# Performance work log

Measured on AMD Instinct MI355X. Metric: run time of the kernel, lower is better.

Reference implementation:

```python
import jax, jax.numpy as jnp
import numpy as np

NUM_ENT = 100000
NUM_REL = 500            # distinct relations; table holds 2*NUM_REL (forward + inverse)
E = 500000               # total edges: first half original, second half reversed
D = 200                  # init_dim = gcn_dim = embed_dim
B = 256
KW, KH = 10, 20          # ConvE reshape: 2*KW*KH == 2*D
NF, KS = 200, 7
FLAT = (2 * KW - KS + 1) * (KH - KS + 1) * NF  # 14*14*200 = 39200
EPS = 1e-5


def setup_inputs() -> dict:
    key = jax.random.key(0)
    k = jax.random.split(key, 24)
    half = E // 2
    src = jax.random.randint(k[0], (half,), 0, NUM_ENT)
    dst = jax.random.randint(k[1], (half,), 0, NUM_ENT)
    et = jax.random.randint(k[2], (half,), 0, NUM_REL)
    edge_index = jnp.stack([jnp.concatenate([src, dst]), jnp.concatenate([dst, src])])
    edge_type = jnp.concatenate([et, et + NUM_REL])
    sub = jax.random.randint(k[3], (B,), 0, NUM_ENT)
    rel = jax.random.randint(k[4], (B,), 0, 2 * NUM_REL)
    g = lambda i, shape, s=0.05: jax.random.normal(k[i], shape, jnp.float32) * s
    return dict(
        sub=sub, rel=rel, edge_index=edge_index, edge_type=edge_type,
        init_embed=g(5, (NUM_ENT, D)), init_rel=g(6, (2 * NUM_REL, D)),
        loop_rel1=g(7, (1, D)), loop_rel2=g(8, (1, D)),
        w_in1=g(9, (D, D)), w_out1=g(10, (D, D)), w_loop1=g(11, (D, D)), w_rel1=g(12, (D, D)), b1=jnp.zeros((D,), jnp.float32),
        w_in2=g(13, (D, D)), w_out2=g(14, (D, D)), w_loop2=g(15, (D, D)), w_rel2=g(16, (D, D)), b2=jnp.zeros((D,), jnp.float32),
        conv_w=g(17, (NF, 1, KS, KS)), conv_b=jnp.zeros((NF,), jnp.float32),
        bn0_g=jnp.ones((1,), jnp.float32), bn0_b=jnp.zeros((1,), jnp.float32),
        bn1_g=jnp.ones((NF,), jnp.float32), bn1_b=jnp.zeros((NF,), jnp.float32),
        bn2_g=jnp.ones((D,), jnp.float32), bn2_b=jnp.zeros((D,), jnp.float32),
        fc_w=g(18, (FLAT, D)), fc_b=jnp.zeros((D,), jnp.float32),
        ent_bias=jnp.zeros((NUM_ENT,), jnp.float32),
    )


def _bn2d(x, g, b):  # eval-mode BN: running mean 0, running var 1
    s = g / jnp.sqrt(1.0 + EPS)
    return x * s[None, :, None, None] + b[None, :, None, None]


def _bn1d(x, g, b):
    return x * (g / jnp.sqrt(1.0 + EPS)) + b


def _agg(x_src, rel_e, dst, w):
    # message = comp(h_src, h_rel) @ W   (subtraction composition), degree-normalized scatter
    m = (x_src - rel_e) @ w                                        # [E/2, D]
    s = jax.ops.segment_sum(m, dst, num_segments=NUM_ENT)          # [N, D]
    deg = jax.ops.segment_sum(jnp.ones(dst.shape, m.dtype), dst, num_segments=NUM_ENT)
    return s / jnp.clip(deg, 1.0)[:, None]


def _ragcn_layer(x, r, ei, et, w_in, w_out, w_loop, w_rel, loop_rel, b):
    half = ei.shape[1] // 2
    src, dst = ei[0], ei[1]
    re = r[et]                                                     # [E, D]
    res = (_agg(x[src[:half]], re[:half], dst[:half], w_in)
           + _agg(x[src[half:]], re[half:], dst[half:], w_out)
           + (x - loop_rel) @ w_loop)
    return jnp.tanh(res / 3.0 + b), r @ w_rel


def _forward(sub, rel, edge_index, edge_type, init_embed, init_rel,
             loop_rel1, loop_rel2, w_in1, w_out1, w_loop1, w_rel1, b1,
             w_in2, w_out2, w_loop2, w_rel2, b2, conv_w, conv_b,
             bn0_g, bn0_b, bn1_g, bn1_b, bn2_g, bn2_b, fc_w, fc_b, ent_bias):
    x, r = _ragcn_layer(init_embed, init_rel, edge_index, edge_type, w_in1, w_out1, w_loop1, w_rel1, loop_rel1, b1)
    x, r = _ragcn_layer(x, r, edge_index, edge_type, w_in2, w_out2, w_loop2, w_rel2, loop_rel2, b2)
    sub_emb = x[sub]                                               # [B, D]
    rel_emb = r[rel]                                               # [B, D]
    # ConvE concat: [B,2,D] -> [B,D,2] -> [B,1,2*KW,KH]
    stk = jnp.transpose(jnp.stack([sub_emb, rel_emb], axis=1), (0, 2, 1)).reshape(-1, 1, 2 * KW, KH)
    h = _bn2d(stk, bn0_g, bn0_b)
    h = jax.lax.conv_general_dilated(h, conv_w, (1, 1), 'VALID',
                                     dimension_numbers=('NCHW', 'OIHW', 'NCHW'))
    h = h + conv_b[None, :, None, None]
    h = jax.nn.relu(_bn2d(h, bn1_g, bn1_b))
    h = h.reshape(-1, FLAT)
    h = h @ fc_w + fc_b
    h = jax.nn.relu(_bn1d(h, bn2_g, bn2_b))
    logits = h @ x.T + ent_bias                                    # [B, NUM_ENT]
    return jax.nn.sigmoid(logits)


def reference(sub, rel, edge_index, edge_type, init_embed, init_rel,
              loop_rel1, loop_rel2, w_in1, w_out1, w_loop1, w_rel1, b1,
              w_in2, w_out2, w_loop2, w_rel2, b2, conv_w, conv_b,
              bn0_g, bn0_b, bn1_g, bn1_b, bn2_g, bn2_b, fc_w, fc_b, ent_bias):
    return _forward(sub, rel, edge_index, edge_type, init_embed, init_rel,
                    loop_rel1, loop_rel2, w_in1, w_out1, w_loop1, w_rel1, b1,
                    w_in2, w_out2, w_loop2, w_rel2, b2, conv_w, conv_b,
                    bn0_g, bn0_b, bn1_g, bn1_b, bn2_g, bn2_b, fc_w, fc_b, ent_bias)
```

## Files before the change

### kernel.cpp

```cpp
#include <hip/hip_runtime.h>
#include <math.h>

#define N_ENT   100000
#define N_REL2  1000
#define E_TOT   500000
#define E_HALF  250000
#define DIM     200
#define BB      256
#define NFILT   200
#define FLATK   39200
#define EPS_BN  1e-5f

#define NROWS   200000
#define SCHUNK  2048
#define SNBLK   ((NROWS + SCHUNK - 1) / SCHUNK)

#define FC_KC   175
#define FC_KLEN 224

typedef __attribute__((ext_vector_type(8))) short bf16x8;
typedef __attribute__((ext_vector_type(4))) float f32x4;

__device__ __forceinline__ unsigned short f2b(float f) {
    union { float f; unsigned u; } c; c.f = f;
    unsigned u = c.u;
    u += 0x7fffu + ((u >> 16) & 1u);
    return (unsigned short)(u >> 16);
}
__device__ __forceinline__ float b2f(unsigned short h) {
    union { unsigned u; float f; } c; c.u = ((unsigned)h) << 16;
    return c.f;
}
__device__ __forceinline__ float fast_tanh(float x) {
    float ax = fabsf(x);
    float e = __expf(-2.0f * ax);
    float t = (1.0f - e) / (1.0f + e);
    return copysignf(t, x);
}

__global__ void convert_kernel(const float* __restrict__ s, unsigned short* __restrict__ d,
                               int n) {
    int i = (blockIdx.x * 256 + threadIdx.x) * 4;
    if (i + 3 < n) {
        float4 v = *(const float4*)(s + i);
        ushort4 o;
        o.x = f2b(v.x); o.y = f2b(v.y); o.z = f2b(v.z); o.w = f2b(v.w);
        *(ushort4*)(d + i) = o;
    } else {
        for (; i < n; ++i) d[i] = f2b(s[i]);
    }
}

__global__ void wstack_kernel(const float* __restrict__ wIn, const float* __restrict__ wOut,
                              const float* __restrict__ wLoop, unsigned short* __restrict__ WT) {
    int g = blockIdx.x * 256 + threadIdx.x;
    if (g >= 224 * 672) return;
    int j = g / 672, t = g - j * 672;
    int seg = t / 224, k = t - seg * 224;
    float v = 0.f;
    if (j < 200 && k < 200)
        v = (seg == 0 ? wIn : seg == 1 ? wOut : wLoop)[k * 200 + j];
    WT[g] = f2b(v);
}

__global__ void fwt_kernel(const float* __restrict__ fw, unsigned short* __restrict__ FWT) {
    __shared__ float t[32][33];
    const int bid = blockIdx.x;
    const int kt = bid % 1225, jt = bid / 1225;
    const int tid = threadIdx.x;
#pragma unroll
    for (int it = 0; it < 4; ++it) {
        int idx = tid + it * 256;
        int kk = idx >> 5, jj = idx & 31;
        int j = jt * 32 + jj;
        t[kk][jj] = (j < 200) ? fw[(size_t)(kt * 32 + kk) * 200 + j] : 0.f;
    }
    __syncthreads();
#pragma unroll
    for (int it = 0; it < 4; ++it) {
        int idx = tid + it * 256;
        int jj = idx >> 5, kk = idx & 31;
        int j = jt * 32 + jj;
        if (j < 208)
            FWT[(size_t)j * FLATK + kt * 32 + kk] = f2b(t[kk][jj]);
    }
}

__global__ void hist_kernel(const int* __restrict__ ei, int* __restrict__ cnt) {
    int e = blockIdx.x * 256 + threadIdx.x;
    if (e >= E_TOT) return;
    int row = ei[E_TOT + e] + (e < E_HALF ? 0 : N_ENT);
    atomicAdd(&cnt[row], 1);
}

__global__ void scan1_kernel(const int* __restrict__ cnt, int* __restrict__ row_start,
                             int* __restrict__ blockSum) {
    __shared__ int tsum[256];
    const int t = threadIdx.x;
    const int base = blockIdx.x * SCHUNK + t * 8;
    int v[8];
    int s = 0;
#pragma unroll
    for (int i = 0; i < 8; ++i) {
        int idx = base + i;
        int c = (idx < NROWS) ? cnt[idx] : 0;
        v[i] = s;
        s += c;
    }
    tsum[t] = s;
    __syncthreads();
    for (int off = 1; off < 256; off <<= 1) {
        int x = (t >= off) ? tsum[t - off] : 0;
        __syncthreads();
        if (t >= off) tsum[t] += x;
        __syncthreads();
    }
    int texc = (t == 0) ? 0 : tsum[t - 1];
    if (t == 0) blockSum[blockIdx.x] = tsum[255];
#pragma unroll
    for (int i = 0; i < 8; ++i) {
        int idx = base + i;
        if (idx < NROWS) row_start[idx] = texc + v[i];
    }
}

__global__ void scan2_kernel(int* __restrict__ blockSum) {
    int s = 0;
    for (int i = 0; i < SNBLK; ++i) { int c = blockSum[i]; blockSum[i] = s; s += c; }
}

__global__ void scan3_kernel(int* __restrict__ row_start, int* __restrict__ row_cur,
                             const int* __restrict__ blockSum) {
    int i = blockIdx.x * 256 + threadIdx.x;
    if (i >= NROWS) return;
    int v = row_start[i] + blockSum[i / SCHUNK];
    row_start[i] = v;
    row_cur[i] = v;
}

__global__ void fill_kernel(const int* __restrict__ ei, const int* __restrict__ et,
                            int* __restrict__ row_cur, int2* __restrict__ epair) {
    int e = blockIdx.x * 256 + threadIdx.x;
    if (e >= E_TOT) return;
    int row = ei[E_TOT + e] + (e < E_HALF ? 0 : N_ENT);
    int pos = atomicAdd(&row_cur[row], 1);
    epair[pos] = make_int2(ei[e], et[e]);
}

__global__ void gather_kernel(const unsigned short* __restrict__ x,
                              const unsigned short* __restrict__ r,
                              const int2* __restrict__ epair,
                              const int* __restrict__ row_start, const int* __restrict__ cnt,
                              unsigned short* __restrict__ agg) {
    int wid = blockIdx.x * 4 + (threadIdx.x >> 6);
    if (wid >= NROWS) return;
    int lane = threadIdx.x & 63;
    if (lane >= 50) return;
    int start = row_start[wid];
    int deg = cnt[wid];
    float a0 = 0.f, a1 = 0.f, a2 = 0.f, a3 = 0.f;
    float c0 = 0.f, c1 = 0.f, c2 = 0.f, c3 = 0.f;
    int i = 0;
    for (; i + 2 <= deg; i += 2) {
        int2 e0 = epair[start + i];
        int2 e1 = epair[start + i + 1];
        ushort4 xv0 = *(const ushort4*)(x + (size_t)e0.x * DIM + lane * 4);
        ushort4 rv0 = *(const ushort4*)(r + (size_t)e0.y * DIM + lane * 4);
        ushort4 xv1 = *(const ushort4*)(x + (size_t)e1.x * DIM + lane * 4);
        ushort4 rv1 = *(const ushort4*)(r + (size_t)e1.y * DIM + lane * 4);
        a0 += b2f(xv0.x) - b2f(rv0.x);
        a1 += b2f(xv0.y) - b2f(rv0.y);
        a2 += b2f(xv0.z) - b2f(rv0.z);
        a3 += b2f(xv0.w) - b2f(rv0.w);
        c0 += b2f(xv1.x) - b2f(rv1.x);
        c1 += b2f(xv1.y) - b2f(rv1.y);
        c2 += b2f(xv1.z) - b2f(rv1.z);
        c3 += b2f(xv1.w) - b2f(rv1.w);
    }
    if (i < deg) {
        int2 e = epair[start + i];
        ushort4 xv = *(const ushort4*)(x + (size_t)e.x * DIM + lane * 4);
        ushort4 rv = *(const ushort4*)(r + (size_t)e.y * DIM + lane * 4);
        a0 += b2f(xv.x) - b2f(rv.x);
        a1 += b2f(xv.y) - b2f(rv.y);
        a2 += b2f(xv.z) - b2f(rv.z);
        a3 += b2f(xv.w) - b2f(rv.w);
    }
    float sc = 1.0f / fmaxf((float)deg, 1.0f);
    ushort4 o;
    o.x = f2b((a0 + c0) * sc);
    o.y = f2b((a1 + c1) * sc);
    o.z = f2b((a2 + c2) * sc);
    o.w = f2b((a3 + c3) * sc);
    *(ushort4*)(agg + (size_t)wid * DIM + lane * 4) = o;
}

__global__ void lv_kernel(const float* __restrict__ lr, const float* __restrict__ wl,
                          float* __restrict__ lv) {
    int j = blockIdx.x * blockDim.x + threadIdx.x;
    if (j >= DIM) return;
    float acc = 0.f;
    for (int k = 0; k < DIM; ++k) acc += lr[k] * wl[k * DIM + j];
    lv[j] = acc;
}

__global__ void rgemm_kernel(const float* __restrict__ r, const float* __restrict__ w,
                             float* __restrict__ out, int rows) {
    int g = blockIdx.x * 256 + threadIdx.x;
    if (g >= rows * DIM) return;
    int i = g / DIM, j = g - i * DIM;
    float acc = 0.f;
    for (int k = 0; k < DIM; ++k) acc += r[i * DIM + k] * w[k * DIM + j];
    out[g] = acc;
}

#define LOAD_A2(g, buf) do {                                                    \
    const unsigned short* Ap_ = Aseg[(g) / 7];                                  \
    const unsigned short* base_ = Ap_ + (size_t)arow * 200 + ((g) % 7) * 32 + lq * 8; \
    buf[0] = *(const bf16x8*)(base_);                                           \
    buf[1] = *(const bf16x8*)(base_ + 16 * 200);                                \
} while (0)

__global__ __launch_bounds__(256, 4) void layer_mfma_kernel(
        const unsigned short* __restrict__ aggI, const unsigned short* __restrict__ aggO,
        const unsigned short* __restrict__ xin, const unsigned short* __restrict__ WT,
        const float* __restrict__ lv, const float* __restrict__ bias,
        unsigned short* __restrict__ out, int nwg) {
    __shared__ unsigned short Wl[112 * 136];
    const int bid = blockIdx.x;
    const int q = nwg >> 3, rr = nwg & 7;
    const int xcd = bid & 7, idx = bid >> 3;
    const int L = (xcd < rr ? xcd * (q + 1) : rr * (q + 1) + (xcd - rr) * q) + idx;
    const int rowblk  = L >> 1;
    const int colbase = (L & 1) * 112;

    const int tid  = threadIdx.x;
    const int wm   = tid >> 6;
    const int lane = tid & 63;
    const int lr   = lane & 15;
    const int lq   = lane >> 4;
    const int row0 = rowblk * 128;
    const int arow = row0 + wm * 32 + lr;

    const unsigned short* const Aseg[3] = { aggI, aggO, xin };

    f32x4 acc[2][7];
#pragma unroll
    for (int m = 0; m < 2; ++m)
#pragma unroll
        for (int n = 0; n < 7; ++n) acc[m][n] = (f32x4){0.f, 0.f, 0.f, 0.f};

    bf16x8 apf[3][2];
    LOAD_A2(0, apf[0]);
    LOAD_A2(1, apf[1]);

#pragma unroll
    for (int seg = 0; seg < 3; ++seg) {
#pragma unroll
        for (int ph = 0; ph < 2; ++ph) {
            if (seg + ph) __syncthreads();
            if (ph == 0) {
#pragma unroll
                for (int it = 0; it < 7; ++it) {
                    int u = tid + it * 256;
                    int col = u >> 4, kq = u & 15;
                    *(int4*)(&Wl[col * 136 + kq * 8]) =
                        *(const int4*)(WT + (size_t)(colbase + col) * 672 + seg * 224 + kq * 8);
                }
            } else {
                for (int u = tid; u < 1344; u += 256) {
                    int col = u / 12, kq = u - col * 12;
                    *(int4*)(&Wl[col * 136 + kq * 8]) =
                        *(const int4*)(WT + (size_t)(colbase + col) * 672 + seg * 224 + 128 + kq * 8);
                }
            }
            __syncthreads();
            const int NC = (ph == 0) ? 4 : 3;
#pragma unroll
            for (int cc = 0; cc < NC; ++cc) {
                const int g = seg * 7 + (ph ? 4 : 0) + cc;
                if (g + 2 < 21) LOAD_A2(g + 2, apf[(g + 2) % 3]);
#pragma unroll
                for (int n = 0; n < 7; ++n) {
                    bf16x8 b = *(const bf16x8*)(&Wl[(n * 16 + lr) * 136 + cc * 32 + lq * 8]);
                    acc[0][n] = __builtin_amdgcn_mfma_f32_16x16x32_bf16(apf[g % 3][0], b, acc[0][n], 0, 0, 0);
                    acc[1][n] = __builtin_amdgcn_mfma_f32_16x16x32_bf16(apf[g % 3][1], b, acc[1][n], 0, 0, 0);
                }
            }
        }
    }

#pragma unroll
    for (int m = 0; m < 2; ++m) {
        int rbase = row0 + wm * 32 + m * 16 + lq * 4;
#pragma unroll
        for (int n = 0; n < 7; ++n) {
            int col = colbase + n * 16 + lr;
            if (col < 200) {
                float lvc = lv[col], bc = bias[col];
#pragma unroll
                for (int r2 = 0; r2 < 4; ++r2) {
                    int row = rbase + r2;
                    if (row < N_ENT) {
                        float v = (acc[m][n][r2] - lvc) * (1.0f / 3.0f) + bc;
                        out[(size_t)row * 200 + col] = f2b(fast_tanh(v));
                    }
                }
            }
        }
    }
}

__global__ void img_kernel(const unsigned short* __restrict__ x, const float* __restrict__ r,
                           const int* __restrict__ sub, const int* __restrict__ rel,
                           const float* __restrict__ bn0g, const float* __restrict__ bn0b,
                           unsigned short* __restrict__ img) {
    int g = blockIdx.x * 256 + threadIdx.x;
    if (g >= BB * 2 * DIM) return;
    int b = g / 400, l = g - b * 400;
    int d = l >> 1;
    float v = (l & 1) ? r[(size_t)rel[b] * DIM + d] : b2f(x[(size_t)sub[b] * DIM + d]);
    float s0 = bn0g[0] * rsqrtf(1.0f + EPS_BN);
    img[g] = f2b(v * s0 + bn0b[0]);
}

__global__ void im2col_kernel(const unsigned short* __restrict__ img,
                              unsigned short* __restrict__ IM) {
    int g = blockIdx.x * 256 + threadIdx.x;
    if (g >= 50176 * 64) return;
    int row = g >> 6, k = g & 63;
    int b = row / 196, p = row - b * 196;
    int h = p / 14, w = p - h * 14;
    unsigned short v = 0;
    if (k < 49) {
        int i = k / 7, j = k - i * 7;
        v = img[b * 400 + (h + i) * 20 + (w + j)];
    }
    IM[g] = v;
}

__global__ void cwt_kernel(const float* __restrict__ cw, unsigned short* __restrict__ CWT) {
    int g = blockIdx.x * 256 + threadIdx.x;
    if (g >= 208 * 64) return;
    int f = g >> 6, k = g & 63;
    CWT[g] = (f < 200 && k < 49) ? f2b(cw[f * 49 + k]) : 0;
}

__global__ __launch_bounds__(256) void conv_mfma_kernel(
        const unsigned short* __restrict__ IM, const unsigned short* __restrict__ CWT,
        const float* __restrict__ cb, const float* __restrict__ bn1g,
        const float* __restrict__ bn1b, unsigned short* __restrict__ CO_B) {
    const int tid  = threadIdx.x;
    const int row0 = blockIdx.x * 128;
    const int wave = tid >> 6;
    const int lane = tid & 63;
    const int lr   = lane & 15;
    const int lq   = lane >> 4;
    const int arow = row0 + wave * 32 + lr;

    f32x4 acc[2][13];
#pragma unroll
    for (int m = 0; m < 2; ++m)
#pragma unroll
        for (int n = 0; n < 13; ++n) acc[m][n] = (f32x4){0.f, 0.f, 0.f, 0.f};

#pragma unroll
    for (int c = 0; c < 2; ++c) {
        const int k = c * 32 + lq * 8;
        bf16x8 a0 = *(const bf16x8*)(IM + (size_t)arow * 64 + k);
        bf16x8 a1 = *(const bf16x8*)(IM + (size_t)(arow + 16) * 64 + k);
#pragma unroll
        for (int n = 0; n < 13; ++n) {
            bf16x8 b = *(const bf16x8*)(CWT + (size_t)(n * 16 + lr) * 64 + k);
            acc[0][n] = __builtin_amdgcn_mfma_f32_16x16x32_bf16(a0, b, acc[0][n], 0, 0, 0);
            acc[1][n] = __builtin_amdgcn_mfma_f32_16x16x32_bf16(a1, b, acc[1][n], 0, 0, 0);
        }
    }

#pragma unroll
    for (int m = 0; m < 2; ++m) {
        int grow_base = row0 + wave * 32 + m * 16 + lq * 4;
#pragma unroll
        for (int n = 0; n < 13; ++n) {
            int col = n * 16 + lr;
            if (col < 200) {
                float s1 = bn1g[col] * rsqrtf(1.0f + EPS_BN);
                float t1 = bn1b[col];
                float cbf = cb[col];
#pragma unroll
                for (int r = 0; r < 4; ++r) {
                    int grow = grow_base + r;
                    int b = grow / 196, p = grow - b * 196;
                    float v = fmaxf((acc[m][n][r] + cbf) * s1 + t1, 0.f);
                    CO_B[(size_t)b * FLATK + col * 196 + p] = f2b(v);
                }
            }
        }
    }
}

__global__ __launch_bounds__(256) void fc_mfma_kernel(
        const unsigned short* __restrict__ CO_B, const unsigned short* __restrict__ FWT,
        float* __restrict__ partials) {
    const int tid  = threadIdx.x;
    const int kc   = blockIdx.x >> 2;
    const int mb   = blockIdx.x & 3;
    const int wave = tid >> 6;
    const int lane = tid & 63;
    const int lr   = lane & 15;
    const int lq   = lane >> 4;
    const int m0   = mb * 64 + wave * 16;

    f32x4 acc[13];
#pragma unroll
    for (int n = 0; n < 13; ++n) acc[n] = (f32x4){0.f, 0.f, 0.f, 0.f};

#pragma unroll
    for (int s = 0; s < 7; ++s) {
        const int k = kc * FC_KLEN + s * 32 + lq * 8;
        bf16x8 a = *(const bf16x8*)(CO_B + (size_t)(m0 + lr) * FLATK + k);
#pragma unroll
        for (int n = 0; n < 13; ++n) {
            bf16x8 b = *(const bf16x8*)(FWT + (size_t)(n * 16 + lr) * FLATK + k);
            acc[n] = __builtin_amdgcn_mfma_f32_16x16x32_bf16(a, b, acc[n], 0, 0, 0);
        }
    }

    float* slab = partials + (size_t)kc * (BB * 208);
#pragma unroll
    for (int n = 0; n < 13; ++n) {
        int col = n * 16 + lr;
#pragma unroll
        for (int r = 0; r < 4; ++r) {
            int row = m0 + lq * 4 + r;
            slab[(size_t)row * 208 + col] = acc[n][r];
        }
    }
}

__global__ void fc_reduce_kernel(const float* __restrict__ partials,
                                 const float* __restrict__ fcb,
                                 const float* __restrict__ g2, const float* __restrict__ b2v,
                                 unsigned short* __restrict__ hb) {
    int g = blockIdx.x * 256 + threadIdx.x;
    if (g >= BB * 224) return;
    int b = g / 224, j = g - b * 224;
    unsigned short o = 0;
    if (j < 200) {
        float s = 0.f;
        const float* p = partials + (size_t)b * 208 + j;
#pragma unroll 5
        for (int c = 0; c < FC_KC; ++c)
            s += p[(size_t)c * (BB * 208)];
        float v = (s + fcb[j]) * (g2[j] * rsqrtf(1.0f + EPS_BN)) + b2v[j];
        o = f2b(fmaxf(v, 0.f));
    }
    hb[g] = o;
}

__global__ __launch_bounds__(256) void logits_mfma_kernel(
        const unsigned short* __restrict__ x, const unsigned short* __restrict__ hb,
        const float* __restrict__ eb, float* __restrict__ out) {
    const int tid  = threadIdx.x;
    const int nb   = blockIdx.x >> 1;
    const int mb   = blockIdx.x & 1;
    const int ent0 = nb * 208;
    const int wave = tid >> 6;
    const int lane = tid & 63;
    const int lr   = lane & 15;
    const int lq   = lane >> 4;
    const int brow = mb * 128 + wave * 32 + lr;

    f32x4 acc[2][13];
#pragma unroll
    for (int m = 0; m < 2; ++m)
#pragma unroll
        for (int n = 0; n < 13; ++n) acc[m][n] = (f32x4){0.f, 0.f, 0.f, 0.f};

#pragma unroll
    for (int c = 0; c < 7; ++c) {
        const int k = c * 32 + lq * 8;
        bf16x8 a0 = *(const bf16x8*)(hb + (size_t)brow * 224 + k);
        bf16x8 a1 = *(const bf16x8*)(hb + (size_t)(brow + 16) * 224 + k);
#pragma unroll
        for (int n = 0; n < 13; ++n) {
            bf16x8 b = *(const bf16x8*)(x + (size_t)(ent0 + n * 16 + lr) * 200 + k);
            acc[0][n] = __builtin_amdgcn_mfma_f32_16x16x32_bf16(a0, b, acc[0][n], 0, 0, 0);
            acc[1][n] = __builtin_amdgcn_mfma_f32_16x16x32_bf16(a1, b, acc[1][n], 0, 0, 0);
        }
    }

#pragma unroll
    for (int m = 0; m < 2; ++m) {
        int b_base = mb * 128 + wave * 32 + m * 16 + lq * 4;
#pragma unroll
        for (int n = 0; n < 13; ++n) {
            int ent = ent0 + n * 16 + lr;
            if (ent < N_ENT) {
                float bias = eb[ent];
#pragma unroll
                for (int r = 0; r < 4; ++r) {
                    float v = acc[m][n][r] + bias;
                    out[(size_t)(b_base + r) * N_ENT + ent] = 1.0f / (1.0f + __expf(-v));
                }
            }
        }
    }
}

extern "C" void kernel_launch(void* const* d_in, const int* in_sizes, int n_in,
                              void* d_out, int out_size, void* d_ws, size_t ws_size,
                              hipStream_t stream) {
    const int*   sub        = (const int*)  d_in[0];
    const int*   rel        = (const int*)  d_in[1];
    const int*   edge_index = (const int*)  d_in[2];
    const int*   edge_type  = (const int*)  d_in[3];
    const float* init_embed = (const float*)d_in[4];
    const float* init_rel   = (const float*)d_in[5];
    const float* loop_rel1  = (const float*)d_in[6];
    const float* loop_rel2  = (const float*)d_in[7];
    const float* w_in1      = (const float*)d_in[8];
    const float* w_out1     = (const float*)d_in[9];
    const float* w_loop1    = (const float*)d_in[10];
    const float* w_rel1     = (const float*)d_in[11];
    const float* b1         = (const float*)d_in[12];
    const float* w_in2      = (const float*)d_in[13];
    const float* w_out2     = (const float*)d_in[14];
    const float* w_loop2    = (const float*)d_in[15];
    const float* w_rel2     = (const float*)d_in[16];
    const float* b2         = (const float*)d_in[17];
    const float* conv_w     = (const float*)d_in[18];
    const float* conv_b     = (const float*)d_in[19];
    const float* bn0_g      = (const float*)d_in[20];
    const float* bn0_b      = (const float*)d_in[21];
    const float* bn1_g      = (const float*)d_in[22];
    const float* bn1_b      = (const float*)d_in[23];
    const float* bn2_g      = (const float*)d_in[24];
    const float* bn2_b      = (const float*)d_in[25];
    const float* fc_w       = (const float*)d_in[26];
    const float* fc_b       = (const float*)d_in[27];
    const float* ent_bias   = (const float*)d_in[28];

    unsigned short* aggb = (unsigned short*)d_ws;
    unsigned short* x0b  = aggb + 40000000;
    unsigned short* x1b  = x0b  + 20000000;
    unsigned short* r0b  = x1b  + 20000000;
    unsigned short* r1b  = r0b  + 200000;
    unsigned short* WT   = r1b  + 200000;
    unsigned short* img  = WT   + 150528;
    unsigned short* IM   = img  + 102400;
    unsigned short* CWT  = IM   + 3211264;
    unsigned short* CO_B = CWT  + 13312;
    unsigned short* hb16 = CO_B + 10035200;
    unsigned short* FWT  = hb16 + 57344;
    float* fbase = (float*)(FWT + 8153600);
    float* r1f      = fbase;
    float* r2f      = r1f  + 200000;
    float* lv       = r2f  + 200000;
    float* partials = lv   + 256;

    int2* epair    = (int2*)CO_B;
    int* cnt       = (int*)(epair + E_TOT);
    int* row_start = cnt  + NROWS;
    int* row_cur   = row_start + NROWS;
    int* blockSum  = row_cur + NROWS;

    unsigned short* aggIb = aggb;
    unsigned short* aggOb = aggb + (size_t)N_ENT * DIM;
    unsigned short* x2b   = x0b;

    const int gather_blocks = (NROWS + 3) / 4;
    const int layer_nwg     = ((N_ENT + 127) / 128) * 2;
    const int wstack_blocks = (224 * 672 + 255) / 256;

    convert_kernel<<<(N_ENT * DIM + 1023) / 1024, 256, 0, stream>>>(init_embed, x0b, N_ENT * DIM);
    convert_kernel<<<(N_REL2 * DIM + 1023) / 1024, 256, 0, stream>>>(init_rel, r0b, N_REL2 * DIM);
    hipMemsetAsync(cnt, 0, (size_t)NROWS * 4, stream);
    hist_kernel<<<(E_TOT + 255) / 256, 256, 0, stream>>>(edge_index, cnt);
    scan1_kernel<<<SNBLK, 256, 0, stream>>>(cnt, row_start, blockSum);
    scan2_kernel<<<1, 1, 0, stream>>>(blockSum);
    scan3_kernel<<<(NROWS + 255) / 256, 256, 0, stream>>>(row_start, row_cur, blockSum);
    fill_kernel<<<(E_TOT + 255) / 256, 256, 0, stream>>>(edge_index, edge_type, row_cur, epair);

    wstack_kernel<<<wstack_blocks, 256, 0, stream>>>(w_in1, w_out1, w_loop1, WT);
    gather_kernel<<<gather_blocks, 256, 0, stream>>>(x0b, r0b, epair, row_start, cnt, aggb);
    lv_kernel<<<1, 256, 0, stream>>>(loop_rel1, w_loop1, lv);
    layer_mfma_kernel<<<layer_nwg, 256, 0, stream>>>(aggIb, aggOb, x0b, WT, lv, b1, x1b, layer_nwg);
    rgemm_kernel<<<(N_REL2 * DIM + 255) / 256, 256, 0, stream>>>(init_rel, w_rel1, r1f, N_REL2);
    convert_kernel<<<(N_REL2 * DIM + 1023) / 1024, 256, 0, stream>>>(r1f, r1b, N_REL2 * DIM);

    wstack_kernel<<<wstack_blocks, 256, 0, stream>>>(w_in2, w_out2, w_loop2, WT);
    gather_kernel<<<gather_blocks, 256, 0, stream>>>(x1b, r1b, epair, row_start, cnt, aggb);
    lv_kernel<<<1, 256, 0, stream>>>(loop_rel2, w_loop2, lv);
    layer_mfma_kernel<<<layer_nwg, 256, 0, stream>>>(aggIb, aggOb, x1b, WT, lv, b2, x2b, layer_nwg);
    rgemm_kernel<<<(N_REL2 * DIM + 255) / 256, 256, 0, stream>>>(r1f, w_rel2, r2f, N_REL2);

    img_kernel<<<(BB * 400 + 255) / 256, 256, 0, stream>>>(x2b, r2f, sub, rel,
                                                           bn0_g, bn0_b, img);
    im2col_kernel<<<(50176 * 64 + 255) / 256, 256, 0, stream>>>(img, IM);
    cwt_kernel<<<(208 * 64 + 255) / 256, 256, 0, stream>>>(conv_w, CWT);
    conv_mfma_kernel<<<50176 / 128, 256, 0, stream>>>(IM, CWT, conv_b, bn1_g, bn1_b, CO_B);
    fwt_kernel<<<1225 * 7, 256, 0, stream>>>(fc_w, FWT);
    fc_mfma_kernel<<<FC_KC * 4, 256, 0, stream>>>(CO_B, FWT, partials);
    fc_reduce_kernel<<<(BB * 224 + 255) / 256, 256, 0, stream>>>(partials, fc_b, bn2_g, bn2_b, hb16);

    logits_mfma_kernel<<<481 * 2, 256, 0, stream>>>(x2b, hb16, ent_bias, (float*)d_out);
}
```

Baseline: 643.1 us.

## Stage entity tiles in LDS for logits GEMM with XCD-aware block mapping

```diff
diff --git a/kernel.cpp b/kernel.cpp
--- a/kernel.cpp
+++ b/kernel.cpp
@@ -458,43 +458,88 @@
     hb[g] = o;
 }
 
-__global__ __launch_bounds__(256) void logits_mfma_kernel(
+#define LOAD_HB(g, buf) do {                                                    \
+    const unsigned short* base_ = hb + (size_t)brow * 224 + (g) * 32 + lq * 8;  \
+    buf[0] = *(const bf16x8*)(base_);                                           \
+    buf[1] = *(const bf16x8*)(base_ + 16 * 224);                                \
+} while (0)
+
+__global__ __launch_bounds__(512, 2) void logits_mfma_kernel(
         const unsigned short* __restrict__ x, const unsigned short* __restrict__ hb,
-        const float* __restrict__ eb, float* __restrict__ out) {
+        const float* __restrict__ eb, float* __restrict__ out, int nwg) {
+    __shared__ unsigned short Xl[112 * 136];
+    const int bid = blockIdx.x;
+    const int q = nwg >> 3, rr = nwg & 7;
+    const int xcd = bid & 7, idx = bid >> 3;
+    const int nb = (xcd < rr ? xcd * (q + 1) : rr * (q + 1) + (xcd - rr) * q) + idx;
+    const int ent0 = nb * 112;
+
     const int tid  = threadIdx.x;
-    const int nb   = blockIdx.x >> 1;
-    const int mb   = blockIdx.x & 1;
-    const int ent0 = nb * 208;
     const int wave = tid >> 6;
+    const int mh   = wave >> 2;
+    const int wm   = wave & 3;
     const int lane = tid & 63;
     const int lr   = lane & 15;
     const int lq   = lane >> 4;
-    const int brow = mb * 128 + wave * 32 + lr;
-
-    f32x4 acc[2][13];
+    const int brow = mh * 128 + wm * 32 + lr;
+
+    f32x4 acc[2][7];
 #pragma unroll
     for (int m = 0; m < 2; ++m)
 #pragma unroll
-        for (int n = 0; n < 13; ++n) acc[m][n] = (f32x4){0.f, 0.f, 0.f, 0.f};
-
-#pragma unroll
-    for (int c = 0; c < 7; ++c) {
-        const int k = c * 32 + lq * 8;
-        bf16x8 a0 = *(const bf16x8*)(hb + (size_t)brow * 224 + k);
-        bf16x8 a1 = *(const bf16x8*)(hb + (size_t)(brow + 16) * 224 + k);
-#pragma unroll
-        for (int n = 0; n < 13; ++n) {
-            bf16x8 b = *(const bf16x8*)(x + (size_t)(ent0 + n * 16 + lr) * 200 + k);
-            acc[0][n] = __builtin_amdgcn_mfma_f32_16x16x32_bf16(a0, b, acc[0][n], 0, 0, 0);
-            acc[1][n] = __builtin_amdgcn_mfma_f32_16x16x32_bf16(a1, b, acc[1][n], 0, 0, 0);
+        for (int n = 0; n < 7; ++n) acc[m][n] = (f32x4){0.f, 0.f, 0.f, 0.f};
+
+    bf16x8 apf[3][2];
+    LOAD_HB(0, apf[0]);
+    LOAD_HB(1, apf[1]);
+
+#pragma unroll
+    for (int ph = 0; ph < 2; ++ph) {
+        if (ph) __syncthreads();
+        if (ph == 0) {
+#pragma unroll
+            for (int it = 0; it < 4; ++it) {
+                int u = tid + it * 512;
+                if (u < 1792) {
+                    int row = u >> 4, c = u & 15;
+                    int ent = ent0 + row;
+                    int4 v = make_int4(0, 0, 0, 0);
+                    if (ent < N_ENT)
+                        v = *(const int4*)(x + (size_t)ent * 200 + c * 8);
+                    *(int4*)(&Xl[row * 136 + c * 8]) = v;
+                }
+            }
+        } else {
+            for (int u = tid; u < 1344; u += 512) {
+                int row = u / 12, c = u - row * 12;
+                int gu = 16 + c;
+                int ent = ent0 + row;
+                int4 v = make_int4(0, 0, 0, 0);
+                if (ent < N_ENT && gu < 25)
+                    v = *(const int4*)(x + (size_t)ent * 200 + gu * 8);
+                *(int4*)(&Xl[row * 136 + c * 8]) = v;
+            }
+        }
+        __syncthreads();
+        const int NC = (ph == 0) ? 4 : 3;
+#pragma unroll
+        for (int cc = 0; cc < NC; ++cc) {
+            const int g = (ph ? 4 : 0) + cc;
+            if (g + 2 < 7) LOAD_HB(g + 2, apf[(g + 2) % 3]);
+#pragma unroll
+            for (int n = 0; n < 7; ++n) {
+                bf16x8 b = *(const bf16x8*)(&Xl[(n * 16 + lr) * 136 + cc * 32 + lq * 8]);
+                acc[0][n] = __builtin_amdgcn_mfma_f32_16x16x32_bf16(apf[g % 3][0], b, acc[0][n], 0, 0, 0);
+                acc[1][n] = __builtin_amdgcn_mfma_f32_16x16x32_bf16(apf[g % 3][1], b, acc[1][n], 0, 0, 0);
+            }
         }
     }
 
 #pragma unroll
     for (int m = 0; m < 2; ++m) {
-        int b_base = mb * 128 + wave * 32 + m * 16 + lq * 4;
-#pragma unroll
-        for (int n = 0; n < 13; ++n) {
+        int b_base = mh * 128 + wm * 32 + m * 16 + lq * 4;
+#pragma unroll
+        for (int n = 0; n < 7; ++n) {
             int ent = ent0 + n * 16 + lr;
             if (ent < N_ENT) {
                 float bias = eb[ent];
@@ -571,6 +616,7 @@
 
     const int gather_blocks = (NROWS + 3) / 4;
     const int layer_nwg     = ((N_ENT + 127) / 128) * 2;
+    const int logits_nwg    = (N_ENT + 111) / 112;
     const int wstack_blocks = (224 * 672 + 255) / 256;
 
     convert_kernel<<<(N_ENT * DIM + 1023) / 1024, 256, 0, stream>>>(init_embed, x0b, N_ENT * DIM);
@@ -604,5 +650,6 @@
     fc_mfma_kernel<<<FC_KC * 4, 256, 0, stream>>>(CO_B, FWT, partials);
     fc_reduce_kernel<<<(BB * 224 + 255) / 256, 256, 0, stream>>>(partials, fc_b, bn2_g, bn2_b, hb16);
 
-    logits_mfma_kernel<<<481 * 2, 256, 0, stream>>>(x2b, hb16, ent_bias, (float*)d_out);
-}
+    logits_mfma_kernel<<<logits_nwg, 512, 0, stream>>>(x2b, hb16, ent_bias, (float*)d_out,
+                                                       logits_nwg);
+}
```

Result: faster. 598.4 us (-7.0%).
